# Optimization experiments

Hardware: AMD Instinct MI355X
Metric: run time of the kernel (lower is better)

Reference implementation:

```python
import jax, jax.numpy as jnp
import numpy as np

B, C, T = 4, 256, 4096
EPS = 1e-5
NEG = -1e8


def setup_inputs() -> dict:
    key = jax.random.key(0)
    ks = jax.random.split(key, 12)
    s = 1.0 / np.sqrt(C)
    x = jax.random.normal(ks[0], (B, C, T), dtype=jnp.float32)
    x_mask = (jax.random.uniform(ks[1], (B, 1, T)) > 0.1).astype(jnp.float32)
    return {
        "x": x,
        "x_mask": x_mask,
        # Normalize params
        "gamma": jnp.ones((C,), jnp.float32),
        "beta": jnp.zeros((C,), jnp.float32),
        "Wp": jax.random.normal(ks[2], (C, C), jnp.float32) * s,
        "bp": jnp.zeros((C,), jnp.float32),
        # 1x1 conv projections (weight [C_out, C_in])
        "Wq": jax.random.normal(ks[3], (C, C), jnp.float32) * s,
        "bq": jnp.zeros((C,), jnp.float32),
        "Wk": jax.random.normal(ks[4], (C, C), jnp.float32) * s,
        "bk": jnp.zeros((C,), jnp.float32),
        "Wv": jax.random.normal(ks[5], (C, C), jnp.float32) * s,
        "bv": jnp.zeros((C,), jnp.float32),
        "Wo": jax.random.normal(ks[6], (C, C), jnp.float32) * s,
        "bo": jnp.zeros((C,), jnp.float32),
    }


def _conv1x1(W, b, x):
    # x: [B, C, T] -> [B, C, T]
    return jnp.einsum('oc,bct->bot', W, x) + b[None, :, None]


def reference(x, x_mask, gamma, beta, Wp, bp, Wq, bq, Wk, bk, Wv, bv, Wo, bo):
    m = x_mask  # [B,1,T]
    h = x * m
    # Normalize: layer_norm over channel dim + linear, operating on [B,T,C]
    ht = h.transpose(0, 2, 1)  # [B,T,C]
    mu = jnp.mean(ht, axis=-1, keepdims=True)
    var = jnp.mean(jnp.square(ht - mu), axis=-1, keepdims=True)
    ln = (ht - mu) * jax.lax.rsqrt(var + EPS) * gamma + beta
    ln = ln @ Wp.T + bp
    h = ln.transpose(0, 2, 1) * m  # [B,C,T]

    q = _conv1x1(Wq, bq, h) * m
    k = _conv1x1(Wk, bk, h) * m
    v = _conv1x1(Wv, bv, h) * m

    scale = float(C) ** (-0.5)
    # scores[b,t,s] = sum_c q[b,c,t] k[b,c,s]
    w = jnp.einsum('bct,bcs->bts', q, k) * scale
    neg = (1.0 - m) * NEG  # [B,1,T]
    w = w + neg + neg.transpose(0, 2, 1)  # mask keys and queries
    w = jax.nn.softmax(w, axis=2)
    # h_[b,c,t] = sum_s v[b,c,s] w[b,t,s]
    h = jnp.einsum('bcs,bts->bct', v, w)
    h = _conv1x1(Wo, bo, h) * m
    return (x + h) * m
```

## Files before the change

kernel.cpp:

```cpp
#include <hip/hip_runtime.h>

#define Bn 4
#define Cn 256
#define Tn 4096

typedef unsigned short u16;
typedef __bf16 bf16x8 __attribute__((ext_vector_type(8)));
typedef float f32x4 __attribute__((ext_vector_type(4)));
typedef float f32x16 __attribute__((ext_vector_type(16)));
typedef u16 u16x8 __attribute__((ext_vector_type(8)));

__device__ __forceinline__ float b2f(u16 u) {
    union { unsigned int i; float f; } v;
    v.i = ((unsigned int)u) << 16;
    return v.f;
}
__device__ __forceinline__ u16 f2b(float f) {
    union { float f; unsigned int i; } v;
    v.f = f;
    unsigned int r = v.i + 0x7FFFu + ((v.i >> 16) & 1u);
    return (u16)(r >> 16);
}
__device__ __forceinline__ bf16x8 ones8() {
    union { u16 u[8]; bf16x8 v; } t;
    for (int j = 0; j < 8; j++) t.u[j] = 0x3F80;
    return t.v;
}

__global__ __launch_bounds__(256) void cvt_kernel(
    const float* __restrict__ w0, const float* __restrict__ w1,
    const float* __restrict__ w2, const float* __restrict__ w3,
    const float* __restrict__ w4, u16* __restrict__ dst)
{
    int gid = blockIdx.x * 256 + threadIdx.x;
    int base = gid * 4;
    int region = base >> 16;
    int off = base & 65535;
    const float* src = region == 0 ? w0 : region == 1 ? w1
                     : region == 2 ? w2 : region == 3 ? w3 : w4;
    float sc = (region == 1) ? 0.0625f : 1.0f;
    float4 v = *(const float4*)(src + off);
    ushort4 o;
    o.x = f2b(v.x * sc); o.y = f2b(v.y * sc);
    o.z = f2b(v.z * sc); o.w = f2b(v.w * sc);
    *(ushort4*)(dst + base) = o;
}

__global__ __launch_bounds__(256) void ln_kernel(
    const float* __restrict__ x, const float* __restrict__ mask,
    const float* __restrict__ gamma, const float* __restrict__ beta,
    u16* __restrict__ lnT)
{
    __shared__ __attribute__((aligned(16))) u16 tile[32][264];
    __shared__ float ssum[8][32], ssq[8][32], smu[32], srs[32];
    const int tid = threadIdx.x;
    const int b = blockIdx.y;
    const int t0 = blockIdx.x * 32;
    const int g = tid >> 5, tl = tid & 31;
    const int t = t0 + tl;
    const float mval = mask[b * Tn + t];
    float s = 0.f, s2 = 0.f;
    for (int c = g; c < Cn; c += 8) {
        float v = x[((size_t)(b * Cn + c)) * Tn + t] * mval;
        s += v; s2 += v * v;
        tile[tl][c] = f2b(v);
    }
    ssum[g][tl] = s; ssq[g][tl] = s2;
    __syncthreads();
    if (tid < 32) {
        float su = 0.f, sq = 0.f;
        for (int k = 0; k < 8; k++) { su += ssum[k][tid]; sq += ssq[k][tid]; }
        float mu = su * (1.f / Cn);
        float var = sq * (1.f / Cn) - mu * mu;
        var = fmaxf(var, 0.0f);
        smu[tid] = mu;
        srs[tid] = 1.0f / sqrtf(var + 1e-5f);
    }
    __syncthreads();
    for (int it = 0; it < 4; it++) {
        int idx = it * 256 + tid;
        int row = idx >> 5, c16 = idx & 31;
        float mu = smu[row], rs = srs[row];
        u16x8 ov;
        for (int j = 0; j < 8; j++) {
            int c = c16 * 8 + j;
            float h = b2f(tile[row][c]);
            float v = (h - mu) * rs * gamma[c] + beta[c];
            ov[j] = f2b(v);
        }
        *(u16x8*)(lnT + ((size_t)(b * Tn + t0 + row)) * Cn + c16 * 8) = ov;
    }
}

__global__ __launch_bounds__(256) void wp_kernel(
    const u16* __restrict__ Xb, const u16* __restrict__ Wb,
    const float* __restrict__ bias, const float* __restrict__ mask,
    u16* __restrict__ Yout)
{
    __shared__ __attribute__((aligned(16))) u16 Al[128][72];
    __shared__ __attribute__((aligned(16))) u16 Bl[64][72];
    const int tid = threadIdx.x;
    const int b = blockIdx.z;
    const int m0 = blockIdx.x * 128;
    const int n0 = blockIdx.y * 64;
    const int wave = tid >> 6, lane = tid & 63;
    const int ln16 = lane & 15, quad = lane >> 4;
    const int wm = (wave & 1) * 64, wn = (wave >> 1) * 32;

    const u16* Abase = Xb + ((size_t)(b * Tn + m0)) * Cn;
    const u16* Bbase = Wb + (size_t)n0 * Cn;

    f32x4 acc[4][2];
    for (int i = 0; i < 4; i++)
        for (int j = 0; j < 2; j++) acc[i][j] = (f32x4){0.f, 0.f, 0.f, 0.f};

    for (int k0 = 0; k0 < Cn; k0 += 64) {
        for (int it = 0; it < 4; it++) {
            int idx = it * 256 + tid;
            int row = idx >> 3, gg = idx & 7;
            *(uint4*)(&Al[row][gg * 8]) =
                *(const uint4*)(Abase + (size_t)row * Cn + k0 + gg * 8);
        }
        for (int it = 0; it < 2; it++) {
            int idx = it * 256 + tid;
            int row = idx >> 3, gg = idx & 7;
            *(uint4*)(&Bl[row][gg * 8]) =
                *(const uint4*)(Bbase + (size_t)row * Cn + k0 + gg * 8);
        }
        __syncthreads();
        for (int kk = 0; kk < 2; kk++) {
            bf16x8 af[4], bfr[2];
            for (int i = 0; i < 4; i++)
                af[i] = *(const bf16x8*)(&Al[wm + i * 16 + ln16][kk * 32 + quad * 8]);
            for (int j = 0; j < 2; j++)
                bfr[j] = *(const bf16x8*)(&Bl[wn + j * 16 + ln16][kk * 32 + quad * 8]);
            for (int i = 0; i < 4; i++)
                for (int j = 0; j < 2; j++)
                    acc[i][j] = __builtin_amdgcn_mfma_f32_16x16x32_bf16(
                        af[i], bfr[j], acc[i][j], 0, 0, 0);
        }
        __syncthreads();
    }
    for (int i = 0; i < 4; i++) {
        for (int j = 0; j < 2; j++) {
            int nn = n0 + wn + j * 16 + ln16;
            for (int r = 0; r < 4; r++) {
                int tt = m0 + wm + i * 16 + quad * 4 + r;
                float val = acc[i][j][r] + bias[nn];
                val *= mask[b * Tn + tt];
                Yout[((size_t)(b * Tn + tt)) * Cn + nn] = f2b(val);
            }
        }
    }
}

__global__ __launch_bounds__(256) void qkv_kernel(
    const u16* __restrict__ h1T,
    const u16* __restrict__ Wq_, const float* __restrict__ bq_,
    const u16* __restrict__ Wk_, const float* __restrict__ bk_,
    const u16* __restrict__ Wv_, const float* __restrict__ bv_,
    const float* __restrict__ mask,
    u16* __restrict__ qO, u16* __restrict__ kO, u16* __restrict__ vO)
{
    __shared__ __attribute__((aligned(16))) u16 Al[128][72];
    __shared__ __attribute__((aligned(16))) u16 Bl[64][72];
    const int tid = threadIdx.x;
    const int z = blockIdx.z;
    const int which = z >> 2;
    const int b = z & 3;
    const u16* W = which == 0 ? Wq_ : which == 1 ? Wk_ : Wv_;
    const float* bi = which == 0 ? bq_ : which == 1 ? bk_ : bv_;
    const float bsc = which == 0 ? 0.0625f : 1.0f;
    const int m0 = blockIdx.x * 128;
    const int n0 = blockIdx.y * 64;
    const int wave = tid >> 6, lane = tid & 63;
    const int ln16 = lane & 15, quad = lane >> 4;
    const int wm = (wave & 1) * 64, wn = (wave >> 1) * 32;

    const u16* Abase = h1T + ((size_t)(b * Tn + m0)) * Cn;
    const u16* Bbase = W + (size_t)n0 * Cn;

    f32x4 acc[4][2];
    for (int i = 0; i < 4; i++)
        for (int j = 0; j < 2; j++) acc[i][j] = (f32x4){0.f, 0.f, 0.f, 0.f};

    for (int k0 = 0; k0 < Cn; k0 += 64) {
        for (int it = 0; it < 4; it++) {
            int idx = it * 256 + tid;
            int row = idx >> 3, gg = idx & 7;
            *(uint4*)(&Al[row][gg * 8]) =
                *(const uint4*)(Abase + (size_t)row * Cn + k0 + gg * 8);
        }
        for (int it = 0; it < 2; it++) {
            int idx = it * 256 + tid;
            int row = idx >> 3, gg = idx & 7;
            *(uint4*)(&Bl[row][gg * 8]) =
                *(const uint4*)(Bbase + (size_t)row * Cn + k0 + gg * 8);
        }
        __syncthreads();
        for (int kk = 0; kk < 2; kk++) {
            bf16x8 af[4], bfr[2];
            for (int i = 0; i < 4; i++)
                af[i] = *(const bf16x8*)(&Al[wm + i * 16 + ln16][kk * 32 + quad * 8]);
            for (int j = 0; j < 2; j++)
                bfr[j] = *(const bf16x8*)(&Bl[wn + j * 16 + ln16][kk * 32 + quad * 8]);
            for (int i = 0; i < 4; i++)
                for (int j = 0; j < 2; j++)
                    acc[i][j] = __builtin_amdgcn_mfma_f32_16x16x32_bf16(
                        af[i], bfr[j], acc[i][j], 0, 0, 0);
        }
        __syncthreads();
    }

    if (which < 2) {
        u16* Yo = which == 0 ? qO : kO;
        for (int i = 0; i < 4; i++) {
            for (int j = 0; j < 2; j++) {
                int nn = n0 + wn + j * 16 + ln16;
                for (int r = 0; r < 4; r++) {
                    int tt = m0 + wm + i * 16 + quad * 4 + r;
                    float val = acc[i][j][r] + bi[nn] * bsc;
                    val *= mask[b * Tn + tt];
                    Yo[((size_t)(b * Tn + tt)) * Cn + nn] = f2b(val);
                }
            }
        }
    } else {
        u16* vt = &Al[0][0];
        for (int i = 0; i < 4; i++) {
            for (int j = 0; j < 2; j++) {
                int nl = wn + j * 16 + ln16;
                for (int r = 0; r < 4; r++) {
                    int ml = wm + i * 16 + quad * 4 + r;
                    int tt = m0 + ml;
                    float val = acc[i][j][r] + bi[n0 + nl];
                    val *= mask[b * Tn + tt];
                    vt[nl * 136 + ml] = f2b(val);
                }
            }
        }
        __syncthreads();
        for (int itc = 0; itc < 4; itc++) {
            int cidx = itc * 256 + tid;
            int row = cidx >> 4;
            int ch = cidx & 15;
            u16x8 ov = *(const u16x8*)(vt + row * 136 + ch * 8);
            *(u16x8*)(vO + ((size_t)(b * Cn + n0 + row)) * Tn + m0 + ch * 8) = ov;
        }
    }
}

__global__ __launch_bounds__(512, 2) void attn_kernel(
    const u16* __restrict__ qT, const u16* __restrict__ kT,
    const u16* __restrict__ vv, const float* __restrict__ mask,
    u16* __restrict__ PO, float* __restrict__ pL)
{
    __shared__ __attribute__((aligned(16))) u16 kls[32][264];
    __shared__ __attribute__((aligned(16))) u16 vls[256][40];
    __shared__ __attribute__((aligned(16))) u16 pls[8][32][40];
    __shared__ float nls[1024];
    const int tid = threadIdx.x;
    const int id = blockIdx.x;
    const int spl = id & 3;
    const int b = (id >> 2) & 3;
    const int qb = id >> 4;
    const int t0 = qb * 256;
    const int wave = tid >> 6, lane = tid & 63;
    const int ln32 = lane & 31, half = lane >> 5;
    const int sBeg = spl * (Tn / 4);

    for (int i = tid; i < 1024; i += 512)
        nls[i] = (1.0f - mask[b * Tn + sBeg + i]) * -1e8f - 8.0f;

    bf16x8 qf[16];
    {
        const u16* qp = qT + ((size_t)(b * Tn + t0 + wave * 32 + ln32)) * Cn + half * 8;
        for (int ks = 0; ks < 16; ks++) qf[ks] = *(const bf16x8*)(qp + ks * 16);
    }
    f32x16 acc[8], lac;
    for (int i = 0; i < 16; i++) lac[i] = 0.f;
    for (int nt = 0; nt < 8; nt++) acc[nt] = lac;
    const bf16x8 ones = ones8();

    const int nIter = (Tn / 4) / 32;

    uint4 kpre[2], vpre[2];
    auto loadK = [&](int s0) {
        for (int i = 0; i < 2; i++) {
            int idx = i * 512 + tid;
            kpre[i] = *(const uint4*)(kT + ((size_t)(b * Tn + s0 + (idx >> 5))) * Cn + (idx & 31) * 8);
        }
    };
    auto loadV = [&](int s0) {
        for (int i = 0; i < 2; i++) {
            int idx = i * 512 + tid;
            vpre[i] = *(const uint4*)(vv + ((size_t)(b * Cn + (idx >> 2))) * Tn + s0 + (idx & 3) * 8);
        }
    };
    loadK(sBeg);
    loadV(sBeg);

    for (int it = 0; it < nIter; it++) {
        const int s0 = sBeg + it * 32;
        __syncthreads();
        for (int i = 0; i < 2; i++) {
            int idx = i * 512 + tid;
            *(uint4*)(&kls[idx >> 5][(idx & 31) * 8]) = kpre[i];
        }
        for (int i = 0; i < 2; i++) {
            int idx = i * 512 + tid;
            *(uint4*)(&vls[idx >> 2][(idx & 3) * 8]) = vpre[i];
        }
        if (it + 1 < nIter) {
            loadK(s0 + 32);
            loadV(s0 + 32);
        }
        __syncthreads();
        const float negk = nls[it * 32 + ln32];

        f32x16 S;
        for (int i = 0; i < 16; i++) S[i] = 0.f;
        for (int ks = 0; ks < 16; ks++) {
            bf16x8 kf = *(const bf16x8*)(&kls[ln32][ks * 16 + half * 8]);
            S = __builtin_amdgcn_mfma_f32_32x32x16_bf16(qf[ks], kf, S, 0, 0, 0);
        }
        for (int r = 0; r < 16; r++) S[r] = __expf(S[r] + negk);
        for (int r = 0; r < 16; r++) {
            int row = (r & 3) + 8 * (r >> 2) + 4 * half;
            pls[wave][row][ln32] = f2b(S[r]);
        }
        bf16x8 pf0 = *(const bf16x8*)(&pls[wave][ln32][half * 8]);
        bf16x8 pf1 = *(const bf16x8*)(&pls[wave][ln32][16 + half * 8]);
        lac = __builtin_amdgcn_mfma_f32_32x32x16_bf16(pf0, ones, lac, 0, 0, 0);
        lac = __builtin_amdgcn_mfma_f32_32x32x16_bf16(pf1, ones, lac, 0, 0, 0);
        for (int nt = 0; nt < 8; nt++) {
            bf16x8 v0 = *(const bf16x8*)(&vls[nt * 32 + ln32][half * 8]);
            bf16x8 v1 = *(const bf16x8*)(&vls[nt * 32 + ln32][16 + half * 8]);
            acc[nt] = __builtin_amdgcn_mfma_f32_32x32x16_bf16(pf0, v0, acc[nt], 0, 0, 0);
            acc[nt] = __builtin_amdgcn_mfma_f32_32x32x16_bf16(pf1, v1, acc[nt], 0, 0, 0);
        }
    }
    const size_t SB = (size_t)spl * (Bn * Tn);
    for (int r = 0; r < 16; r++) {
        int trow = (r & 3) + 8 * (r >> 2) + 4 * half;
        int t = t0 + wave * 32 + trow;
        for (int nt = 0; nt < 8; nt++)
            PO[(SB + b * Tn + t) * Cn + nt * 32 + ln32] = f2b(acc[nt][r]);
        if (ln32 == 0) pL[SB + b * Tn + t] = lac[r];
    }
}

__global__ __launch_bounds__(256) void final_kernel(
    const u16* __restrict__ WoB, const float* __restrict__ bo,
    const u16* __restrict__ PO, const float* __restrict__ pL,
    const float* __restrict__ mask, const float* __restrict__ x,
    float* __restrict__ out)
{
    __shared__ __attribute__((aligned(16))) u16 Al[128][72];
    __shared__ __attribute__((aligned(16))) u16 Bl[64][72];
    __shared__ float rls[64];
    const int tid = threadIdx.x;
    const int b = blockIdx.z;
    const int m0 = blockIdx.x * 128;
    const int n0 = blockIdx.y * 64;
    const int wave = tid >> 6, lane = tid & 63;
    const int ln16 = lane & 15, quad = lane >> 4;
    const int wm = (wave & 1) * 64, wn = (wave >> 1) * 32;
    const size_t BT = (size_t)Bn * Tn;

    if (tid < 64) {
        size_t R = (size_t)b * Tn + n0 + tid;
        float l = pL[R] + pL[BT + R] + pL[2 * BT + R] + pL[3 * BT + R];
        rls[tid] = 1.0f / fmaxf(l, 1e-30f);
    }

    f32x4 acc[4][2];
    for (int i = 0; i < 4; i++)
        for (int j = 0; j < 2; j++) acc[i][j] = (f32x4){0.f, 0.f, 0.f, 0.f};

    for (int k0 = 0; k0 < Cn; k0 += 64) {
        for (int it = 0; it < 4; it++) {
            int idx = it * 256 + tid;
            int row = idx >> 3, gg = idx & 7;
            *(uint4*)(&Al[row][gg * 8]) =
                *(const uint4*)(WoB + (size_t)(m0 + row) * Cn + k0 + gg * 8);
        }
        for (int it = 0; it < 2; it++) {
            int idx = it * 256 + tid;
            int row = idx >> 3, gg = idx & 7;
            size_t base = ((size_t)b * Tn + n0 + row) * Cn + k0 + gg * 8;
            u16x8 a0 = *(const u16x8*)(PO + base);
            u16x8 a1 = *(const u16x8*)(PO + BT * Cn + base);
            u16x8 a2 = *(const u16x8*)(PO + 2 * BT * Cn + base);
            u16x8 a3 = *(const u16x8*)(PO + 3 * BT * Cn + base);
            u16x8 o;
            for (int j = 0; j < 8; j++)
                o[j] = f2b(b2f(a0[j]) + b2f(a1[j]) + b2f(a2[j]) + b2f(a3[j]));
            *(u16x8*)(&Bl[row][gg * 8]) = o;
        }
        __syncthreads();
        for (int kk = 0; kk < 2; kk++) {
            bf16x8 af[4], bfr[2];
            for (int i = 0; i < 4; i++)
                af[i] = *(const bf16x8*)(&Al[wm + i * 16 + ln16][kk * 32 + quad * 8]);
            for (int j = 0; j < 2; j++)
                bfr[j] = *(const bf16x8*)(&Bl[wn + j * 16 + ln16][kk * 32 + quad * 8]);
            for (int i = 0; i < 4; i++)
                for (int j = 0; j < 2; j++)
                    acc[i][j] = __builtin_amdgcn_mfma_f32_16x16x32_bf16(
                        af[i], bfr[j], acc[i][j], 0, 0, 0);
        }
        __syncthreads();
    }
    for (int i = 0; i < 4; i++) {
        for (int j = 0; j < 2; j++) {
            int nl = wn + j * 16 + ln16;
            int tt = n0 + nl;
            float rl = rls[nl];
            float mk = mask[b * Tn + tt];
            for (int r = 0; r < 4; r++) {
                int oo = m0 + wm + i * 16 + quad * 4 + r;
                float val = acc[i][j][r] * rl + bo[oo];
                float xr = x[((size_t)(b * Cn + oo)) * Tn + tt];
                out[((size_t)(b * Cn + oo)) * Tn + tt] = (xr + val * mk) * mk;
            }
        }
    }
}

extern "C" void kernel_launch(void* const* d_in, const int* in_sizes, int n_in,
                              void* d_out, int out_size, void* d_ws, size_t ws_size,
                              hipStream_t stream)
{
    const float* x     = (const float*)d_in[0];
    const float* xmask = (const float*)d_in[1];
    const float* gamma = (const float*)d_in[2];
    const float* beta  = (const float*)d_in[3];
    const float* Wp = (const float*)d_in[4];
    const float* bp = (const float*)d_in[5];
    const float* Wq = (const float*)d_in[6];
    const float* bq = (const float*)d_in[7];
    const float* Wk = (const float*)d_in[8];
    const float* bk = (const float*)d_in[9];
    const float* Wv = (const float*)d_in[10];
    const float* bv = (const float*)d_in[11];
    const float* Wo = (const float*)d_in[12];
    const float* bo = (const float*)d_in[13];
    float* out = (float*)d_out;

    u16* ws = (u16*)d_ws;
    const size_t SZ = (size_t)Bn * Tn * Cn;
    const size_t WSZ = (size_t)Cn * Cn;
    u16* lnT = ws;
    u16* h1T = ws + SZ;
    u16* qTt = ws + 2 * SZ;
    u16* kTt = ws + 3 * SZ;
    u16* vB  = ws + 4 * SZ;
    u16* wbf = ws + 5 * SZ;
    u16* PO  = ws + 5 * SZ + 5 * WSZ;
    float* pL = (float*)(PO + 4 * SZ);

    u16* WpB = wbf;
    u16* WqB = wbf + WSZ;
    u16* WkB = wbf + 2 * WSZ;
    u16* WvB = wbf + 3 * WSZ;
    u16* WoB = wbf + 4 * WSZ;

    dim3 blk(256);
    cvt_kernel<<<dim3(320), blk, 0, stream>>>(Wp, Wq, Wk, Wv, Wo, wbf);
    ln_kernel<<<dim3(Tn / 32, Bn), blk, 0, stream>>>(x, xmask, gamma, beta, lnT);
    wp_kernel<<<dim3(Tn / 128, Cn / 64, Bn), blk, 0, stream>>>(
        lnT, WpB, bp, xmask, h1T);
    qkv_kernel<<<dim3(Tn / 128, Cn / 64, 3 * Bn), blk, 0, stream>>>(
        h1T, WqB, bq, WkB, bk, WvB, bv, xmask, qTt, kTt, vB);
    attn_kernel<<<dim3(256), dim3(512), 0, stream>>>(qTt, kTt, vB, xmask, PO, pL);
    final_kernel<<<dim3(Cn / 128, Tn / 64, Bn), blk, 0, stream>>>(
        WoB, bo, PO, pL, xmask, x, out);
}
```

Measured before the change: 268.4 us.

## Pair waves to share P tiles in PV and defer PV one iteration

The attention kernel now groups waves into pairs. Each wave computes PV for 64 query rows against half of the 256 value channels, reading both waves' P tiles from shared memory, so each V fragment is reused across two M-tiles. PV for the previous key block is deferred into the next iteration before the barrier, using a double-buffered V tile, so it can overlap the global prefetch and the QK work. This adds shared memory for the second V buffer and cross-wave P reads, and depends on the barrier placement to keep the pls buffers coherent.

```diff
diff --git a/kernel.cpp b/kernel.cpp
--- a/kernel.cpp
+++ b/kernel.cpp
@@ -256,7 +256,7 @@
     u16* __restrict__ PO, float* __restrict__ pL)
 {
     __shared__ __attribute__((aligned(16))) u16 kls[32][264];
-    __shared__ __attribute__((aligned(16))) u16 vls[256][40];
+    __shared__ __attribute__((aligned(16))) u16 vls[2][256][40];
     __shared__ __attribute__((aligned(16))) u16 pls[8][32][40];
     __shared__ float nls[1024];
     const int tid = threadIdx.x;
@@ -267,6 +267,7 @@
     const int t0 = qb * 256;
     const int wave = tid >> 6, lane = tid & 63;
     const int ln32 = lane & 31, half = lane >> 5;
+    const int pair = wave >> 1, sub = wave & 1;
     const int sBeg = spl * (Tn / 4);
 
     for (int i = tid; i < 1024; i += 512)
@@ -274,7 +275,7 @@
 
     bf16x8 qf[16];
     {
-        const u16* qp = qT + ((size_t)(b * Tn + t0 + wave * 32 + ln32)) * Cn + half * 8;
+        const u16* qp = qT + ((size_t)(b * Tn + t0 + pair * 64 + sub * 32 + ln32)) * Cn + half * 8;
         for (int ks = 0; ks < 16; ks++) qf[ks] = *(const bf16x8*)(qp + ks * 16);
     }
     f32x16 acc[8], lac;
@@ -297,11 +298,32 @@
             vpre[i] = *(const uint4*)(vv + ((size_t)(b * Cn + (idx >> 2))) * Tn + s0 + (idx & 3) * 8);
         }
     };
+    auto pv = [&](int pb) {
+        bf16x8 pf[2][2];
+        for (int mt = 0; mt < 2; mt++) {
+            int wsrc = pair * 2 + mt;
+            pf[mt][0] = *(const bf16x8*)(&pls[wsrc][ln32][half * 8]);
+            pf[mt][1] = *(const bf16x8*)(&pls[wsrc][ln32][16 + half * 8]);
+        }
+        for (int nt = 0; nt < 4; nt++) {
+            int cb = sub * 128 + nt * 32 + ln32;
+            bf16x8 v0 = *(const bf16x8*)(&vls[pb][cb][half * 8]);
+            bf16x8 v1 = *(const bf16x8*)(&vls[pb][cb][16 + half * 8]);
+            acc[nt]     = __builtin_amdgcn_mfma_f32_32x32x16_bf16(pf[0][0], v0, acc[nt], 0, 0, 0);
+            acc[nt]     = __builtin_amdgcn_mfma_f32_32x32x16_bf16(pf[0][1], v1, acc[nt], 0, 0, 0);
+            acc[4 + nt] = __builtin_amdgcn_mfma_f32_32x32x16_bf16(pf[1][0], v0, acc[4 + nt], 0, 0, 0);
+            acc[4 + nt] = __builtin_amdgcn_mfma_f32_32x32x16_bf16(pf[1][1], v1, acc[4 + nt], 0, 0, 0);
+        }
+        lac = __builtin_amdgcn_mfma_f32_32x32x16_bf16(pf[sub][0], ones, lac, 0, 0, 0);
+        lac = __builtin_amdgcn_mfma_f32_32x32x16_bf16(pf[sub][1], ones, lac, 0, 0, 0);
+    };
+
     loadK(sBeg);
     loadV(sBeg);
 
     for (int it = 0; it < nIter; it++) {
         const int s0 = sBeg + it * 32;
+        const int cb = it & 1;
         __syncthreads();
         for (int i = 0; i < 2; i++) {
             int idx = i * 512 + tid;
@@ -309,12 +331,13 @@
         }
         for (int i = 0; i < 2; i++) {
             int idx = i * 512 + tid;
-            *(uint4*)(&vls[idx >> 2][(idx & 3) * 8]) = vpre[i];
+            *(uint4*)(&vls[cb][idx >> 2][(idx & 3) * 8]) = vpre[i];
         }
         if (it + 1 < nIter) {
             loadK(s0 + 32);
             loadV(s0 + 32);
         }
+        if (it) pv(1 - cb);
         __syncthreads();
         const float negk = nls[it * 32 + ln32];
 
@@ -329,24 +352,23 @@
             int row = (r & 3) + 8 * (r >> 2) + 4 * half;
             pls[wave][row][ln32] = f2b(S[r]);
         }
-        bf16x8 pf0 = *(const bf16x8*)(&pls[wave][ln32][half * 8]);
-        bf16x8 pf1 = *(const bf16x8*)(&pls[wave][ln32][16 + half * 8]);
-        lac = __builtin_amdgcn_mfma_f32_32x32x16_bf16(pf0, ones, lac, 0, 0, 0);
-        lac = __builtin_amdgcn_mfma_f32_32x32x16_bf16(pf1, ones, lac, 0, 0, 0);
-        for (int nt = 0; nt < 8; nt++) {
-            bf16x8 v0 = *(const bf16x8*)(&vls[nt * 32 + ln32][half * 8]);
-            bf16x8 v1 = *(const bf16x8*)(&vls[nt * 32 + ln32][16 + half * 8]);
-            acc[nt] = __builtin_amdgcn_mfma_f32_32x32x16_bf16(pf0, v0, acc[nt], 0, 0, 0);
-            acc[nt] = __builtin_amdgcn_mfma_f32_32x32x16_bf16(pf1, v1, acc[nt], 0, 0, 0);
-        }
-    }
+    }
+    __syncthreads();
+    pv((nIter - 1) & 1);
+
     const size_t SB = (size_t)spl * (Bn * Tn);
     for (int r = 0; r < 16; r++) {
         int trow = (r & 3) + 8 * (r >> 2) + 4 * half;
-        int t = t0 + wave * 32 + trow;
-        for (int nt = 0; nt < 8; nt++)
-            PO[(SB + b * Tn + t) * Cn + nt * 32 + ln32] = f2b(acc[nt][r]);
-        if (ln32 == 0) pL[SB + b * Tn + t] = lac[r];
+        for (int mt = 0; mt < 2; mt++) {
+            int t = t0 + pair * 64 + mt * 32 + trow;
+            for (int nt = 0; nt < 4; nt++)
+                PO[(SB + b * Tn + t) * Cn + sub * 128 + nt * 32 + ln32] =
+                    f2b(acc[mt * 4 + nt][r]);
+        }
+        if (ln32 == 0) {
+            int t = t0 + pair * 64 + sub * 32 + trow;
+            pL[SB + b * Tn + t] = lac[r];
+        }
     }
 }
 
```

Result: slower. 427.8 us (+59.4%).

## Raise attention key-split factor to eight when workspace allows

Applied to the files above, without the earlier changes.

Makes the split-K (key dimension) factor of the attention kernel a runtime parameter and picks 8 splits instead of 4 when the workspace is large enough. This doubles the grid from 256 to 512 blocks to fill more CUs on the MI355X. To find room, it reuses the lnT/h1T buffers, which are dead by then, for two of the partial-output slabs. The final kernel now sums a variable number of bf16 partials, which adds global traffic for the extra partial outputs and a longer reduction loop.

```diff
diff --git a/kernel.cpp b/kernel.cpp
--- a/kernel.cpp
+++ b/kernel.cpp
@@ -253,7 +253,8 @@
 __global__ __launch_bounds__(512, 2) void attn_kernel(
     const u16* __restrict__ qT, const u16* __restrict__ kT,
     const u16* __restrict__ vv, const float* __restrict__ mask,
-    u16* __restrict__ PO, float* __restrict__ pL)
+    u16* __restrict__ PO01, u16* __restrict__ POx, float* __restrict__ pL,
+    int sshift)
 {
     __shared__ __attribute__((aligned(16))) u16 kls[32][264];
     __shared__ __attribute__((aligned(16))) u16 vls[256][40];
@@ -261,15 +262,18 @@
     __shared__ float nls[1024];
     const int tid = threadIdx.x;
     const int id = blockIdx.x;
-    const int spl = id & 3;
-    const int b = (id >> 2) & 3;
-    const int qb = id >> 4;
+    const int split = 1 << sshift;
+    const int spl = id & (split - 1);
+    const int b = (id >> sshift) & 3;
+    const int qb = id >> (sshift + 2);
     const int t0 = qb * 256;
     const int wave = tid >> 6, lane = tid & 63;
     const int ln32 = lane & 31, half = lane >> 5;
-    const int sBeg = spl * (Tn / 4);
-
-    for (int i = tid; i < 1024; i += 512)
+    const int sLen = Tn >> sshift;
+    const int sBeg = spl * sLen;
+    const int nIter = sLen >> 5;
+
+    for (int i = tid; i < sLen; i += 512)
         nls[i] = (1.0f - mask[b * Tn + sBeg + i]) * -1e8f - 8.0f;
 
     bf16x8 qf[16];
@@ -281,8 +285,6 @@
     for (int i = 0; i < 16; i++) lac[i] = 0.f;
     for (int nt = 0; nt < 8; nt++) acc[nt] = lac;
     const bf16x8 ones = ones8();
-
-    const int nIter = (Tn / 4) / 32;
 
     uint4 kpre[2], vpre[2];
     auto loadK = [&](int s0) {
@@ -340,21 +342,24 @@
             acc[nt] = __builtin_amdgcn_mfma_f32_32x32x16_bf16(pf1, v1, acc[nt], 0, 0, 0);
         }
     }
-    const size_t SB = (size_t)spl * (Bn * Tn);
+    const size_t SZe = (size_t)Bn * Tn * Cn;
+    u16* myPO = (spl < 2) ? PO01 + (size_t)spl * SZe
+                          : POx + (size_t)(spl - 2) * SZe;
     for (int r = 0; r < 16; r++) {
         int trow = (r & 3) + 8 * (r >> 2) + 4 * half;
         int t = t0 + wave * 32 + trow;
         for (int nt = 0; nt < 8; nt++)
-            PO[(SB + b * Tn + t) * Cn + nt * 32 + ln32] = f2b(acc[nt][r]);
-        if (ln32 == 0) pL[SB + b * Tn + t] = lac[r];
+            myPO[((size_t)(b * Tn + t)) * Cn + nt * 32 + ln32] = f2b(acc[nt][r]);
+        if (ln32 == 0) pL[(size_t)spl * (Bn * Tn) + b * Tn + t] = lac[r];
     }
 }
 
 __global__ __launch_bounds__(256) void final_kernel(
     const u16* __restrict__ WoB, const float* __restrict__ bo,
-    const u16* __restrict__ PO, const float* __restrict__ pL,
+    const u16* __restrict__ PO01, const u16* __restrict__ POx,
+    const float* __restrict__ pL,
     const float* __restrict__ mask, const float* __restrict__ x,
-    float* __restrict__ out)
+    float* __restrict__ out, int split)
 {
     __shared__ __attribute__((aligned(16))) u16 Al[128][72];
     __shared__ __attribute__((aligned(16))) u16 Bl[64][72];
@@ -367,10 +372,12 @@
     const int ln16 = lane & 15, quad = lane >> 4;
     const int wm = (wave & 1) * 64, wn = (wave >> 1) * 32;
     const size_t BT = (size_t)Bn * Tn;
+    const size_t SZe = BT * Cn;
 
     if (tid < 64) {
         size_t R = (size_t)b * Tn + n0 + tid;
-        float l = pL[R] + pL[BT + R] + pL[2 * BT + R] + pL[3 * BT + R];
+        float l = 0.f;
+        for (int p = 0; p < split; p++) l += pL[p * BT + R];
         rls[tid] = 1.0f / fmaxf(l, 1e-30f);
     }
 
@@ -389,13 +396,15 @@
             int idx = it * 256 + tid;
             int row = idx >> 3, gg = idx & 7;
             size_t base = ((size_t)b * Tn + n0 + row) * Cn + k0 + gg * 8;
-            u16x8 a0 = *(const u16x8*)(PO + base);
-            u16x8 a1 = *(const u16x8*)(PO + BT * Cn + base);
-            u16x8 a2 = *(const u16x8*)(PO + 2 * BT * Cn + base);
-            u16x8 a3 = *(const u16x8*)(PO + 3 * BT * Cn + base);
+            float s8[8] = {0.f, 0.f, 0.f, 0.f, 0.f, 0.f, 0.f, 0.f};
+            for (int p = 0; p < split; p++) {
+                const u16* Pb = (p < 2) ? PO01 + (size_t)p * SZe
+                                        : POx + (size_t)(p - 2) * SZe;
+                u16x8 a = *(const u16x8*)(Pb + base);
+                for (int j = 0; j < 8; j++) s8[j] += b2f(a[j]);
+            }
             u16x8 o;
-            for (int j = 0; j < 8; j++)
-                o[j] = f2b(b2f(a0[j]) + b2f(a1[j]) + b2f(a2[j]) + b2f(a3[j]));
+            for (int j = 0; j < 8; j++) o[j] = f2b(s8[j]);
             *(u16x8*)(&Bl[row][gg * 8]) = o;
         }
         __syncthreads();
@@ -451,20 +460,29 @@
     u16* ws = (u16*)d_ws;
     const size_t SZ = (size_t)Bn * Tn * Cn;
     const size_t WSZ = (size_t)Cn * Cn;
+    const size_t BT = (size_t)Bn * Tn;
     u16* lnT = ws;
     u16* h1T = ws + SZ;
     u16* qTt = ws + 2 * SZ;
     u16* kTt = ws + 3 * SZ;
     u16* vB  = ws + 4 * SZ;
     u16* wbf = ws + 5 * SZ;
-    u16* PO  = ws + 5 * SZ + 5 * WSZ;
-    float* pL = (float*)(PO + 4 * SZ);
+    u16* PO01 = ws;
+    u16* POx  = ws + 5 * SZ + 5 * WSZ;
 
     u16* WpB = wbf;
     u16* WqB = wbf + WSZ;
     u16* WkB = wbf + 2 * WSZ;
     u16* WvB = wbf + 3 * WSZ;
     u16* WoB = wbf + 4 * WSZ;
+
+    auto need = [&](int split) {
+        return (5 * SZ + 5 * WSZ + (size_t)(split - 2) * SZ) * 2
+             + (size_t)split * BT * 4;
+    };
+    const int sshift = (ws_size >= need(8)) ? 3 : 2;
+    const int split = 1 << sshift;
+    float* pL = (float*)(POx + (size_t)(split - 2) * SZ);
 
     dim3 blk(256);
     cvt_kernel<<<dim3(320), blk, 0, stream>>>(Wp, Wq, Wk, Wv, Wo, wbf);
@@ -473,7 +491,8 @@
         lnT, WpB, bp, xmask, h1T);
     qkv_kernel<<<dim3(Tn / 128, Cn / 64, 3 * Bn), blk, 0, stream>>>(
         h1T, WqB, bq, WkB, bk, WvB, bv, xmask, qTt, kTt, vB);
-    attn_kernel<<<dim3(256), dim3(512), 0, stream>>>(qTt, kTt, vB, xmask, PO, pL);
+    attn_kernel<<<dim3(64 * split), dim3(512), 0, stream>>>(
+        qTt, kTt, vB, xmask, PO01, POx, pL, sshift);
     final_kernel<<<dim3(Cn / 128, Tn / 64, Bn), blk, 0, stream>>>(
-        WoB, bo, PO, pL, xmask, x, out);
-}
+        WoB, bo, PO01, POx, pL, xmask, x, out, split);
+}
```

Result: slower. 277.9 us (+3.5%).

## Double-buffer attention K/V tiles, reuse workspace for partials, keep bf16 residual

Applied to the files above, without the earlier changes.

The attention kernel now double-buffers its K and V LDS tiles by iteration parity, which removes one block barrier per key step. Two of the four split-K partial outputs are placed in workspace that held the layer-norm and projection intermediates, which are dead by then. The layer-norm kernel also writes a masked bf16 copy of x, and the final kernel reads that smaller residual instead of fp32 x. The residual mask multiply is simplified to match. This lowers residual precision and adds an extra write in the layer-norm kernel, in exchange for halving the residual read.

```diff
diff --git a/kernel.cpp b/kernel.cpp
--- a/kernel.cpp
+++ b/kernel.cpp
@@ -49,7 +49,7 @@
 __global__ __launch_bounds__(256) void ln_kernel(
     const float* __restrict__ x, const float* __restrict__ mask,
     const float* __restrict__ gamma, const float* __restrict__ beta,
-    u16* __restrict__ lnT)
+    u16* __restrict__ lnT, u16* __restrict__ xb)
 {
     __shared__ __attribute__((aligned(16))) u16 tile[32][264];
     __shared__ float ssum[8][32], ssq[8][32], smu[32], srs[32];
@@ -63,7 +63,9 @@
     for (int c = g; c < Cn; c += 8) {
         float v = x[((size_t)(b * Cn + c)) * Tn + t] * mval;
         s += v; s2 += v * v;
-        tile[tl][c] = f2b(v);
+        u16 vb = f2b(v);
+        tile[tl][c] = vb;
+        xb[((size_t)(b * Cn + c)) * Tn + t] = vb;
     }
     ssum[g][tl] = s; ssq[g][tl] = s2;
     __syncthreads();
@@ -253,10 +255,10 @@
 __global__ __launch_bounds__(512, 2) void attn_kernel(
     const u16* __restrict__ qT, const u16* __restrict__ kT,
     const u16* __restrict__ vv, const float* __restrict__ mask,
-    u16* __restrict__ PO, float* __restrict__ pL)
-{
-    __shared__ __attribute__((aligned(16))) u16 kls[32][264];
-    __shared__ __attribute__((aligned(16))) u16 vls[256][40];
+    u16* __restrict__ PO01, u16* __restrict__ POx, float* __restrict__ pL)
+{
+    __shared__ __attribute__((aligned(16))) u16 kls[2][32][264];
+    __shared__ __attribute__((aligned(16))) u16 vls[2][256][40];
     __shared__ __attribute__((aligned(16))) u16 pls[8][32][40];
     __shared__ float nls[1024];
     const int tid = threadIdx.x;
@@ -268,6 +270,7 @@
     const int wave = tid >> 6, lane = tid & 63;
     const int ln32 = lane & 31, half = lane >> 5;
     const int sBeg = spl * (Tn / 4);
+    const int nIter = (Tn / 4) / 32;
 
     for (int i = tid; i < 1024; i += 512)
         nls[i] = (1.0f - mask[b * Tn + sBeg + i]) * -1e8f - 8.0f;
@@ -281,8 +284,6 @@
     for (int i = 0; i < 16; i++) lac[i] = 0.f;
     for (int nt = 0; nt < 8; nt++) acc[nt] = lac;
     const bf16x8 ones = ones8();
-
-    const int nIter = (Tn / 4) / 32;
 
     uint4 kpre[2], vpre[2];
     auto loadK = [&](int s0) {
@@ -302,14 +303,14 @@
 
     for (int it = 0; it < nIter; it++) {
         const int s0 = sBeg + it * 32;
-        __syncthreads();
+        const int cb = it & 1;
         for (int i = 0; i < 2; i++) {
             int idx = i * 512 + tid;
-            *(uint4*)(&kls[idx >> 5][(idx & 31) * 8]) = kpre[i];
+            *(uint4*)(&kls[cb][idx >> 5][(idx & 31) * 8]) = kpre[i];
         }
         for (int i = 0; i < 2; i++) {
             int idx = i * 512 + tid;
-            *(uint4*)(&vls[idx >> 2][(idx & 3) * 8]) = vpre[i];
+            *(uint4*)(&vls[cb][idx >> 2][(idx & 3) * 8]) = vpre[i];
         }
         if (it + 1 < nIter) {
             loadK(s0 + 32);
@@ -321,7 +322,7 @@
         f32x16 S;
         for (int i = 0; i < 16; i++) S[i] = 0.f;
         for (int ks = 0; ks < 16; ks++) {
-            bf16x8 kf = *(const bf16x8*)(&kls[ln32][ks * 16 + half * 8]);
+            bf16x8 kf = *(const bf16x8*)(&kls[cb][ln32][ks * 16 + half * 8]);
             S = __builtin_amdgcn_mfma_f32_32x32x16_bf16(qf[ks], kf, S, 0, 0, 0);
         }
         for (int r = 0; r < 16; r++) S[r] = __expf(S[r] + negk);
@@ -334,26 +335,29 @@
         lac = __builtin_amdgcn_mfma_f32_32x32x16_bf16(pf0, ones, lac, 0, 0, 0);
         lac = __builtin_amdgcn_mfma_f32_32x32x16_bf16(pf1, ones, lac, 0, 0, 0);
         for (int nt = 0; nt < 8; nt++) {
-            bf16x8 v0 = *(const bf16x8*)(&vls[nt * 32 + ln32][half * 8]);
-            bf16x8 v1 = *(const bf16x8*)(&vls[nt * 32 + ln32][16 + half * 8]);
+            bf16x8 v0 = *(const bf16x8*)(&vls[cb][nt * 32 + ln32][half * 8]);
+            bf16x8 v1 = *(const bf16x8*)(&vls[cb][nt * 32 + ln32][16 + half * 8]);
             acc[nt] = __builtin_amdgcn_mfma_f32_32x32x16_bf16(pf0, v0, acc[nt], 0, 0, 0);
             acc[nt] = __builtin_amdgcn_mfma_f32_32x32x16_bf16(pf1, v1, acc[nt], 0, 0, 0);
         }
     }
-    const size_t SB = (size_t)spl * (Bn * Tn);
+    const size_t SZe = (size_t)Bn * Tn * Cn;
+    u16* myPO = (spl < 2) ? PO01 + (size_t)spl * SZe
+                          : POx + (size_t)(spl - 2) * SZe;
     for (int r = 0; r < 16; r++) {
         int trow = (r & 3) + 8 * (r >> 2) + 4 * half;
         int t = t0 + wave * 32 + trow;
         for (int nt = 0; nt < 8; nt++)
-            PO[(SB + b * Tn + t) * Cn + nt * 32 + ln32] = f2b(acc[nt][r]);
-        if (ln32 == 0) pL[SB + b * Tn + t] = lac[r];
+            myPO[((size_t)(b * Tn + t)) * Cn + nt * 32 + ln32] = f2b(acc[nt][r]);
+        if (ln32 == 0) pL[(size_t)spl * (Bn * Tn) + b * Tn + t] = lac[r];
     }
 }
 
 __global__ __launch_bounds__(256) void final_kernel(
     const u16* __restrict__ WoB, const float* __restrict__ bo,
-    const u16* __restrict__ PO, const float* __restrict__ pL,
-    const float* __restrict__ mask, const float* __restrict__ x,
+    const u16* __restrict__ PO01, const u16* __restrict__ POx,
+    const float* __restrict__ pL,
+    const float* __restrict__ mask, const u16* __restrict__ xb,
     float* __restrict__ out)
 {
     __shared__ __attribute__((aligned(16))) u16 Al[128][72];
@@ -367,6 +371,7 @@
     const int ln16 = lane & 15, quad = lane >> 4;
     const int wm = (wave & 1) * 64, wn = (wave >> 1) * 32;
     const size_t BT = (size_t)Bn * Tn;
+    const size_t SZe = BT * Cn;
 
     if (tid < 64) {
         size_t R = (size_t)b * Tn + n0 + tid;
@@ -389,10 +394,10 @@
             int idx = it * 256 + tid;
             int row = idx >> 3, gg = idx & 7;
             size_t base = ((size_t)b * Tn + n0 + row) * Cn + k0 + gg * 8;
-            u16x8 a0 = *(const u16x8*)(PO + base);
-            u16x8 a1 = *(const u16x8*)(PO + BT * Cn + base);
-            u16x8 a2 = *(const u16x8*)(PO + 2 * BT * Cn + base);
-            u16x8 a3 = *(const u16x8*)(PO + 3 * BT * Cn + base);
+            u16x8 a0 = *(const u16x8*)(PO01 + base);
+            u16x8 a1 = *(const u16x8*)(PO01 + SZe + base);
+            u16x8 a2 = *(const u16x8*)(POx + base);
+            u16x8 a3 = *(const u16x8*)(POx + SZe + base);
             u16x8 o;
             for (int j = 0; j < 8; j++)
                 o[j] = f2b(b2f(a0[j]) + b2f(a1[j]) + b2f(a2[j]) + b2f(a3[j]));
@@ -421,8 +426,8 @@
             for (int r = 0; r < 4; r++) {
                 int oo = m0 + wm + i * 16 + quad * 4 + r;
                 float val = acc[i][j][r] * rl + bo[oo];
-                float xr = x[((size_t)(b * Cn + oo)) * Tn + tt];
-                out[((size_t)(b * Cn + oo)) * Tn + tt] = (xr + val * mk) * mk;
+                float xr = b2f(xb[((size_t)(b * Cn + oo)) * Tn + tt]);
+                out[((size_t)(b * Cn + oo)) * Tn + tt] = (xr + val) * mk;
             }
         }
     }
@@ -451,14 +456,17 @@
     u16* ws = (u16*)d_ws;
     const size_t SZ = (size_t)Bn * Tn * Cn;
     const size_t WSZ = (size_t)Cn * Cn;
+    const size_t BT = (size_t)Bn * Tn;
     u16* lnT = ws;
     u16* h1T = ws + SZ;
     u16* qTt = ws + 2 * SZ;
     u16* kTt = ws + 3 * SZ;
     u16* vB  = ws + 4 * SZ;
     u16* wbf = ws + 5 * SZ;
-    u16* PO  = ws + 5 * SZ + 5 * WSZ;
-    float* pL = (float*)(PO + 4 * SZ);
+    u16* PO01 = ws;
+    u16* POx  = ws + 5 * SZ + 5 * WSZ;
+    float* pL = (float*)(POx + 2 * SZ);
+    u16* xb   = (u16*)(pL + 4 * BT);
 
     u16* WpB = wbf;
     u16* WqB = wbf + WSZ;
@@ -468,12 +476,13 @@
 
     dim3 blk(256);
     cvt_kernel<<<dim3(320), blk, 0, stream>>>(Wp, Wq, Wk, Wv, Wo, wbf);
-    ln_kernel<<<dim3(Tn / 32, Bn), blk, 0, stream>>>(x, xmask, gamma, beta, lnT);
+    ln_kernel<<<dim3(Tn / 32, Bn), blk, 0, stream>>>(x, xmask, gamma, beta, lnT, xb);
     wp_kernel<<<dim3(Tn / 128, Cn / 64, Bn), blk, 0, stream>>>(
         lnT, WpB, bp, xmask, h1T);
     qkv_kernel<<<dim3(Tn / 128, Cn / 64, 3 * Bn), blk, 0, stream>>>(
         h1T, WqB, bq, WkB, bk, WvB, bv, xmask, qTt, kTt, vB);
-    attn_kernel<<<dim3(256), dim3(512), 0, stream>>>(qTt, kTt, vB, xmask, PO, pL);
+    attn_kernel<<<dim3(256), dim3(512), 0, stream>>>(
+        qTt, kTt, vB, xmask, PO01, POx, pL);
     final_kernel<<<dim3(Cn / 128, Tn / 64, Bn), blk, 0, stream>>>(
-        WoB, bo, PO, pL, xmask, x, out);
-}
+        WoB, bo, PO01, POx, pL, xmask, xb, out);
+}
```

New measurement: 246.2 us. 1.09x faster.
